# Optimization experiments

Hardware: AMD Instinct MI355X
Metric: run time of the kernel (lower is better)

## Reference

```python
import jax, jax.numpy as jnp
import numpy as np
from jax import lax

DN = ('NCHW', 'OIHW', 'NCHW')

def _conv(x, w, b):
    # Conv2d(k=4, stride=2, padding=1): H -> H/2
    y = lax.conv_general_dilated(x, w, (2, 2), ((1, 1), (1, 1)), dimension_numbers=DN)
    return y + b[None, :, None, None]

def _deconv(x, w, b):
    # ConvTranspose2d(k=4, stride=2, padding=1): H -> 2H.
    # Equivalent dense conv: flip kernel spatially, swap in/out channels,
    # lhs_dilation = stride, padding = k-1-p = 2.
    wf = jnp.flip(w, (2, 3)).transpose(1, 0, 2, 3)  # (out, in, 4, 4)
    y = lax.conv_general_dilated(x, wf, (1, 1), ((2, 2), (2, 2)), lhs_dilation=(2, 2), dimension_numbers=DN)
    return y + b[None, :, None, None]

def setup_inputs() -> dict:
    key = jax.random.key(0)
    ks = jax.random.split(key, 20)
    f = jnp.float32
    s = 0.05  # small init scale for stability
    inp = {
        'x':   jax.random.uniform(ks[0], (64, 3, 224, 224), dtype=f),
        # encoder conv weights (OIHW) + biases
        'ew1': jax.random.normal(ks[1], (32, 3, 4, 4), f) * s,   'eb1': jnp.zeros((32,), f),
        'ew2': jax.random.normal(ks[2], (64, 32, 4, 4), f) * s,  'eb2': jnp.zeros((64,), f),
        'ew3': jax.random.normal(ks[3], (128, 64, 4, 4), f) * s, 'eb3': jnp.zeros((128,), f),
        'ew4': jax.random.normal(ks[4], (64, 128, 4, 4), f) * s, 'eb4': jnp.zeros((64,), f),
        # codebook: uniform(-1/K, 1/K) like torch init, K=4000, D=12544
        'emb': jax.random.uniform(ks[5], (4000, 12544), f, -1.0 / 4000, 1.0 / 4000),
        # decoder conv-transpose weights in torch layout (in, out, kh, kw) + biases
        'dw1': jax.random.normal(ks[6], (64, 128, 4, 4), f) * s, 'db1': jnp.zeros((128,), f),
        'dw2': jax.random.normal(ks[7], (128, 64, 4, 4), f) * s, 'db2': jnp.zeros((64,), f),
        'dw3': jax.random.normal(ks[8], (64, 32, 4, 4), f) * s,  'db3': jnp.zeros((32,), f),
        'dw4': jax.random.normal(ks[9], (32, 3, 4, 4), f) * s,   'db4': jnp.zeros((3,), f),
    }
    return inp

def reference(x, ew1, eb1, ew2, eb2, ew3, eb3, ew4, eb4, emb,
              dw1, db1, dw2, db2, dw3, db3, dw4, db4):
    sg = lax.stop_gradient
    B = x.shape[0]
    # ---- Encoder ----
    h = jax.nn.relu(_conv(x, ew1, eb1))
    h = jax.nn.relu(_conv(h, ew2, eb2))
    h = jax.nn.relu(_conv(h, ew3, eb3))
    h = _conv(h, ew4, eb4)                 # (B, 64, 14, 14)
    z = h.reshape(B, -1)                   # (B, 12544)
    # ---- Vector quantization ----
    # ||z||^2 - 2 z E^T + ||e||^2, argmin over codebook
    dist = (jnp.sum(z * z, axis=1, keepdims=True)
            - 2.0 * (z @ emb.T)
            + jnp.sum(emb * emb, axis=1))  # (B, 4000)
    idx = jnp.argmin(dist, axis=1)         # (B,)
    quantized = emb[idx]                   # (B, 12544) -- direct gather (== onehot @ emb)
    e_latent = jnp.mean((sg(quantized) - z) ** 2)
    q_latent = jnp.mean((quantized - sg(z)) ** 2)
    vq_loss = q_latent + 0.25 * e_latent
    zq = z + sg(quantized - z)             # straight-through
    # ---- Decoder ----
    d = zq.reshape(B, 64, 14, 14)
    d = jax.nn.relu(_deconv(d, dw1, db1))
    d = jax.nn.relu(_deconv(d, dw2, db2))
    d = jax.nn.relu(_deconv(d, dw3, db3))
    x_recon = jax.nn.sigmoid(_deconv(d, dw4, db4))  # (B, 3, 224, 224)
    recon_loss = jnp.mean((x_recon - x) ** 2)
    loss = recon_loss + vq_loss
    return (x_recon, loss, recon_loss, vq_loss)
```

## Files before the change

### kernel.cpp

```cpp
#include <hip/hip_runtime.h>
#include <math.h>

typedef unsigned short u16;
typedef unsigned int u32;
typedef __attribute__((ext_vector_type(8))) short short8;
typedef __attribute__((ext_vector_type(4))) float f32x4;

__device__ __forceinline__ u16 f2bf(float f) {
    u32 u = __float_as_uint(f);
    u = u + 0x7fffu + ((u >> 16) & 1u);
    return (u16)(u >> 16);
}
__device__ __forceinline__ float bf2f(u16 h) { return __uint_as_float(((u32)h) << 16); }

__device__ __forceinline__ f32x4 mfma16(short8 a, short8 b, f32x4 c) {
    return __builtin_amdgcn_mfma_f32_16x16x32_bf16(a, b, c, 0, 0, 0);
}

__device__ __forceinline__ uint4 pack8(float4 a, float4 b) {
    uint4 r;
    r.x = (u32)f2bf(a.x) | ((u32)f2bf(a.y) << 16);
    r.y = (u32)f2bf(a.z) | ((u32)f2bf(a.w) << 16);
    r.z = (u32)f2bf(b.x) | ((u32)f2bf(b.y) << 16);
    r.w = (u32)f2bf(b.z) | ((u32)f2bf(b.w) << 16);
    return r;
}

#define GLOAD_LDS16(gsrc, ldst)                                                      \
    __builtin_amdgcn_global_load_lds(                                                \
        (__attribute__((address_space(1))) u32*)(gsrc),                              \
        (__attribute__((address_space(3))) u32*)(ldst), 16, 0, 0)

__device__ __forceinline__ void prep1_item(const float* __restrict__ w,
                                           u16* __restrict__ o, int i)
{
    int j = i & 7; int kx = j >> 1, cp = j & 1;
    int r = i >> 3;
    int co = r & 31; int r2 = r >> 5;
    int ky = r2 & 3; int h = r2 >> 2;
    int ci = 2 * h + cp;
    o[i] = (ci < 3) ? f2bf(w[((co * 3 + ci) * 16) + ky * 4 + kx]) : (u16)0;
}
__device__ __forceinline__ void prepc_item(const float* __restrict__ w,
                                           u16* __restrict__ o, int CIN, int COUT, int i)
{
    int j = i & 7; int r = i >> 3;
    int co = r % COUT; int r2 = r / COUT;
    int tap = r2 & 15; int ch = r2 >> 4;
    int ci = ch * 8 + j;
    o[i] = f2bf(w[((size_t)co * CIN + ci) * 16 + tap]);
}
__device__ __forceinline__ void prepd_item(const float* __restrict__ w,
                                           u16* __restrict__ o, int CIN, int COUT,
                                           int COPAD, int i)
{
    int j = i & 7; int r = i >> 3;
    int co = r % COPAD; int r2 = r / COPAD;
    int t16 = r2 & 15; int ch = r2 >> 4;
    int py = t16 >> 3, px = (t16 >> 2) & 1, qq = t16 & 3;
    int ta = qq >> 1, tb = qq & 1;
    int ky = py + 2 * ta, kx = px + 2 * tb;
    int ci = ch * 8 + j;
    o[i] = (co < COUT) ? f2bf(w[(((size_t)ci * COUT + co) * 16) + ky * 4 + kx]) : (u16)0;
}

__global__ __launch_bounds__(256) void prep_all(
    const float* __restrict__ ew1, const float* __restrict__ ew2,
    const float* __restrict__ ew3, const float* __restrict__ ew4,
    const float* __restrict__ dw1, const float* __restrict__ dw2,
    const float* __restrict__ dw3, const float* __restrict__ dw4,
    u16* __restrict__ w1c, u16* __restrict__ wc2,
    u16* __restrict__ wc3, u16* __restrict__ wc4,
    u16* __restrict__ wd1, u16* __restrict__ wd2,
    u16* __restrict__ wd3, u16* __restrict__ wd4)
{
    int i = blockIdx.x * 256 + threadIdx.x;
    if (i < 2048) { prep1_item(ew1, w1c, i); return; }
    i -= 2048;
    if (i < 32768)  { prepc_item(ew2, wc2, 32, 64, i); return; }
    i -= 32768;
    if (i < 131072) { prepc_item(ew3, wc3, 64, 128, i); return; }
    i -= 131072;
    if (i < 131072) { prepc_item(ew4, wc4, 128, 64, i); return; }
    i -= 131072;
    if (i < 131072) { prepd_item(dw1, wd1, 64, 128, 128, i); return; }
    i -= 131072;
    if (i < 131072) { prepd_item(dw2, wd2, 128, 64, 64, i); return; }
    i -= 131072;
    if (i < 32768)  { prepd_item(dw3, wd3, 64, 32, 32, i); return; }
    i -= 32768;
    if (i < 8192)   { prepd_item(dw4, wd4, 32, 3, 16, i); return; }
}

template<int CIN, int COUT, int COTILE, int H2, int W2, int NSEG, int MB,
         int MBW, int NWF, int RELU, int STOREZ>
__global__ __launch_bounds__(256) void conv_mfma(
    const u16* __restrict__ in, const u16* __restrict__ wcvt,
    const float* __restrict__ bias, u16* __restrict__ outp,
    float* __restrict__ z32)
{
    constexpr int CHUNKS = CIN / 8, CGI = CIN / 8, CGO = COUT / 8;
    constexpr int HIN = H2 * 2, WIN = W2 * 2, SLOTW = 35;
    constexpr int NF = COTILE / 16, WM = MB / MBW, WN = NF / NWF;
    static_assert(WM * WN == 4, "wave layout");
    constexpr int TBu = MB * 4 * SLOTW, WBu = 16 * COTILE;
    constexpr int EBu = (MB * 16 * COTILE * 2 + 15) / 16;
    constexpr int SM = (TBu + WBu) > EBu ? (TBu + WBu) : EBu;
    __shared__ uint4 smem[SM];
    uint4* T = smem; uint4* wS = smem + TBu;
    u16* E = (u16*)smem;

    const int tid = threadIdx.x, wid = tid >> 6, lane = tid & 63;
    const int q = lane >> 4, lm = lane & 15;
    const int wm = wid / WN, wn = wid % WN;
    const int cobase = blockIdx.y * COTILE;
    const int mbase = blockIdx.x * MB;

    f32x4 acc[MBW][NWF];
    #pragma unroll
    for (int a = 0; a < MBW; ++a)
        #pragma unroll
        for (int b = 0; b < NWF; ++b) {
            acc[a][b][0] = 0.f; acc[a][b][1] = 0.f;
            acc[a][b][2] = 0.f; acc[a][b][3] = 0.f;
        }

    for (int ch = 0; ch < CHUNKS; ++ch) {
        __syncthreads();
        for (int ib = 0; ib < TBu; ib += 256) {
            int i = ib + tid;
            uint4* ldst = T + ib + (wid << 6);
            if (i < TBu) {
                int mb = i / (4 * SLOTW), r2 = i % (4 * SLOTW);
                int r = r2 / SLOTW, s = r2 % SLOTW;
                int mbg = mbase + mb;
                int n = mbg / (H2 * NSEG), rr = mbg % (H2 * NSEG);
                int oy = rr / NSEG, ox0 = (rr % NSEG) << 4;
                int iy = 2 * oy - 1 + r, ix = 2 * ox0 - 1 + s;
                if ((unsigned)iy < (unsigned)HIN && (unsigned)ix < (unsigned)WIN) {
                    GLOAD_LDS16(in + (size_t)(((n * CGI + ch) * HIN + iy) * WIN + ix) * 8, ldst);
                } else {
                    uint4 zz = {0u, 0u, 0u, 0u};
                    T[i] = zz;
                }
            }
        }
        for (int ib = 0; ib < WBu; ib += 256) {
            int i = ib + tid;
            int tap = i / COTILE, co = i % COTILE;
            GLOAD_LDS16(wcvt + (size_t)((ch * 16 + tap) * COUT + cobase + co) * 8,
                        wS + ib + (wid << 6));
        }
        __syncthreads();
        #pragma unroll
        for (int ky = 0; ky < 4; ++ky) {
            short8 Af[MBW]; short8 Bf[NWF];
            #pragma unroll
            for (int im = 0; im < MBW; ++im) {
                int mb = wm * MBW + im;
                Af[im] = *(const short8*)(T + (mb * 4 + ky) * SLOTW + 2 * lm + q);
            }
            #pragma unroll
            for (int inf = 0; inf < NWF; ++inf)
                Bf[inf] = *(const short8*)(wS + (ky * 4 + q) * COTILE + wn * NWF * 16 + inf * 16 + lm);
            #pragma unroll
            for (int im = 0; im < MBW; ++im)
                #pragma unroll
                for (int inf = 0; inf < NWF; ++inf)
                    acc[im][inf] = mfma16(Af[im], Bf[inf], acc[im][inf]);
        }
    }
    __syncthreads();
    #pragma unroll
    for (int inf = 0; inf < NWF; ++inf) {
        int col = wn * NWF * 16 + inf * 16 + lm;
        float bv = bias[cobase + col];
        #pragma unroll
        for (int im = 0; im < MBW; ++im) {
            int pixb = (wm * MBW + im) * 16 + q * 4;
            #pragma unroll
            for (int r = 0; r < 4; ++r) {
                float v = acc[im][inf][r] + bv;
                if (RELU) v = fmaxf(v, 0.f);
                E[(pixb + r) * COTILE + col] = f2bf(v);
            }
        }
    }
    __syncthreads();
    for (int i = tid; i < MB * 16 * (COTILE / 8); i += 256) {
        int pix = i / (COTILE / 8), cg = i % (COTILE / 8);
        int mb = pix >> 4, m = pix & 15;
        int mbg = mbase + mb;
        int n = mbg / (H2 * NSEG), rr = mbg % (H2 * NSEG);
        int oy = rr / NSEG, ox0 = (rr % NSEG) << 4;
        int ox = ox0 + m;
        if (ox < W2)
            *(uint4*)(outp + (size_t)(((n * CGO + cobase / 8 + cg) * H2 + oy) * W2 + ox) * 8) =
                *(uint4*)(E + pix * COTILE + cg * 8);
    }
    if (STOREZ) {
        for (int i = tid; i < MB * 16 * COTILE; i += 256) {
            int pix = i / COTILE, co = i % COTILE;
            int mb = pix >> 4, m = pix & 15;
            int mbg = mbase + mb;
            int n = mbg / (H2 * NSEG), rr = mbg % (H2 * NSEG);
            int oy = rr / NSEG, ox0 = (rr % NSEG) << 4;
            int ox = ox0 + m;
            if (ox < W2)
                z32[(size_t)((n * COUT + cobase + co) * H2 + oy) * W2 + ox] =
                    bf2f(E[pix * COTILE + co]);
        }
    }
}

__global__ __launch_bounds__(256) void conv1_mfma(
    const float* __restrict__ x, const u16* __restrict__ w1c,
    const float* __restrict__ bias, u16* __restrict__ outp)
{
    constexpr int MB = 16, MBW = 4, NWF = 2, COTILE = 32, W2 = 112, H2 = 112, NSEG = 7;
    constexpr int TBu = MB * 2 * 64, WBu = 256;
    __shared__ uint4 smem[TBu + WBu];
    uint4* T1 = smem; uint4* w1S = smem + TBu;
    u16* E = (u16*)smem;

    const int tid = threadIdx.x, wid = tid >> 6, lane = tid & 63;
    const int q = lane >> 4, lm = lane & 15;
    const int wm = wid;
    const int mbase = blockIdx.x * MB;

    f32x4 acc[MBW][NWF];
    #pragma unroll
    for (int a = 0; a < MBW; ++a)
        #pragma unroll
        for (int b = 0; b < NWF; ++b) {
            acc[a][b][0] = 0.f; acc[a][b][1] = 0.f;
            acc[a][b][2] = 0.f; acc[a][b][3] = 0.f;
        }

    for (int i = tid; i < TBu; i += 256) {
        int mb = i >> 7; int r = i & 127;
        int h = r >> 6; int r2 = r & 63;
        int ky = r2 >> 4; int m = r2 & 15;
        int mbg = mbase + mb;
        int n = mbg / (H2 * NSEG), rr = mbg % (H2 * NSEG);
        int oy = rr / NSEG, ox0 = (rr % NSEG) << 4;
        int iy = 2 * oy - 1 + ky;
        int ixb = 2 * (ox0 + m) - 1;
        u32 u[4];
        #pragma unroll
        for (int kx = 0; kx < 4; ++kx) {
            float v0 = 0.f, v1 = 0.f;
            int ix = ixb + kx;
            if ((unsigned)iy < 224u && (unsigned)ix < 224u) {
                int ci0 = 2 * h;
                v0 = x[((size_t)(n * 3 + ci0) * 224 + iy) * 224 + ix];
                if (ci0 + 1 < 3) v1 = x[((size_t)(n * 3 + ci0 + 1) * 224 + iy) * 224 + ix];
            }
            u[kx] = (u32)f2bf(v0) | ((u32)f2bf(v1) << 16);
        }
        uint4 vv; vv.x = u[0]; vv.y = u[1]; vv.z = u[2]; vv.w = u[3];
        T1[i] = vv;
    }
    if (tid < 256) {
        w1S[tid] = *(const uint4*)(w1c + (size_t)tid * 8);
    }
    __syncthreads();
    #pragma unroll
    for (int h = 0; h < 2; ++h) {
        short8 Af[MBW]; short8 Bf[NWF];
        #pragma unroll
        for (int im = 0; im < MBW; ++im) {
            int mb = wm * MBW + im;
            Af[im] = *(const short8*)(T1 + (mb * 2 + h) * 64 + lane);
        }
        #pragma unroll
        for (int inf = 0; inf < NWF; ++inf)
            Bf[inf] = *(const short8*)(w1S + (h * 4 + q) * 32 + inf * 16 + lm);
        #pragma unroll
        for (int im = 0; im < MBW; ++im)
            #pragma unroll
            for (int inf = 0; inf < NWF; ++inf)
                acc[im][inf] = mfma16(Af[im], Bf[inf], acc[im][inf]);
    }
    __syncthreads();
    #pragma unroll
    for (int inf = 0; inf < NWF; ++inf) {
        int col = inf * 16 + lm;
        float bv = bias[col];
        #pragma unroll
        for (int im = 0; im < MBW; ++im) {
            int pixb = (wm * MBW + im) * 16 + q * 4;
            #pragma unroll
            for (int r = 0; r < 4; ++r) {
                float v = fmaxf(acc[im][inf][r] + bv, 0.f);
                E[(pixb + r) * COTILE + col] = f2bf(v);
            }
        }
    }
    __syncthreads();
    for (int i = tid; i < MB * 16 * (COTILE / 8); i += 256) {
        int pix = i / (COTILE / 8), cg = i % (COTILE / 8);
        int mb = pix >> 4, m = pix & 15;
        int mbg = mbase + mb;
        int n = mbg / (H2 * NSEG), rr = mbg % (H2 * NSEG);
        int oy = rr / NSEG, ox0 = (rr % NSEG) << 4;
        int ox = ox0 + m;
        *(uint4*)(outp + (size_t)(((n * 4 + cg) * H2 + oy) * W2 + ox) * 8) =
            *(uint4*)(E + pix * COTILE + cg * 8);
    }
}

template<int CIN, int COUT, int COPAD, int COTILE, int Hp, int Wp, int NSEG,
         int MB, int MBW, int NWF, int RELU>
__global__ __launch_bounds__(256) void deconv_mfma(
    const u16* __restrict__ in, const u16* __restrict__ dcvt,
    const float* __restrict__ bias, u16* __restrict__ outp)
{
    constexpr int CHUNKS = CIN / 8, CGI = CIN / 8, CGO = COUT / 8;
    constexpr int SLOTW = 17;
    constexpr int NF = COTILE / 16, WM = MB / MBW, WN = NF / NWF;
    static_assert(WM * WN == 4, "wave layout");
    constexpr int BPP = 64 * Hp * NSEG / MB;
    constexpr int TBu = MB * 2 * SLOTW, WBu = 4 * COTILE;
    constexpr int EBu = (MB * 16 * COTILE * 2 + 15) / 16;
    constexpr int SM = (TBu + WBu) > EBu ? (TBu + WBu) : EBu;
    __shared__ uint4 smem[SM];
    uint4* T = smem; uint4* wS = smem + TBu;
    u16* E = (u16*)smem;

    const int tid = threadIdx.x, wid = tid >> 6, lane = tid & 63;
    const int q = lane >> 4, lm = lane & 15;
    const int wm = wid / WN, wn = wid % WN;
    const int par = blockIdx.x / BPP;
    const int py = par >> 1, px = par & 1;
    const int mbase = (blockIdx.x % BPP) * MB;
    const int cobase = blockIdx.y * COTILE;

    f32x4 acc[MBW][NWF];
    #pragma unroll
    for (int a = 0; a < MBW; ++a)
        #pragma unroll
        for (int b = 0; b < NWF; ++b) {
            acc[a][b][0] = 0.f; acc[a][b][1] = 0.f;
            acc[a][b][2] = 0.f; acc[a][b][3] = 0.f;
        }

    for (int ch = 0; ch < CHUNKS; ++ch) {
        __syncthreads();
        for (int ib = 0; ib < TBu; ib += 256) {
            int i = ib + tid;
            uint4* ldst = T + ib + (wid << 6);
            if (i < TBu) {
                int mb = i / (2 * SLOTW), r2 = i % (2 * SLOTW);
                int rr_ = r2 / SLOTW, s = r2 % SLOTW;
                int mbg = mbase + mb;
                int n = mbg / (Hp * NSEG), rm = mbg % (Hp * NSEG);
                int oyp = rm / NSEG, u0 = (rm % NSEG) << 4;
                int iy = oyp + (1 - py) - 1 + rr_;
                int ix = u0 + (1 - px) - 1 + s;
                if ((unsigned)iy < (unsigned)Hp && (unsigned)ix < (unsigned)Wp) {
                    GLOAD_LDS16(in + (size_t)(((n * CGI + ch) * Hp + iy) * Wp + ix) * 8, ldst);
                } else {
                    uint4 zz = {0u, 0u, 0u, 0u};
                    T[i] = zz;
                }
            }
        }
        for (int ib = 0; ib < WBu; ib += 256) {
            int i = ib + tid;
            if (i < WBu) {
                int qq = i / COTILE, co = i % COTILE;
                GLOAD_LDS16(dcvt + (size_t)((ch * 16 + par * 4 + qq) * COPAD + cobase + co) * 8,
                            wS + ib + (wid << 6));
            }
        }
        __syncthreads();
        {
            short8 Af[MBW]; short8 Bf[NWF];
            #pragma unroll
            for (int im = 0; im < MBW; ++im) {
                int mb = wm * MBW + im;
                Af[im] = *(const short8*)(T + (mb * 2 + (1 - (q >> 1))) * SLOTW + lm + 1 - (q & 1));
            }
            #pragma unroll
            for (int inf = 0; inf < NWF; ++inf)
                Bf[inf] = *(const short8*)(wS + q * COTILE + wn * NWF * 16 + inf * 16 + lm);
            #pragma unroll
            for (int im = 0; im < MBW; ++im)
                #pragma unroll
                for (int inf = 0; inf < NWF; ++inf)
                    acc[im][inf] = mfma16(Af[im], Bf[inf], acc[im][inf]);
        }
    }
    __syncthreads();
    #pragma unroll
    for (int inf = 0; inf < NWF; ++inf) {
        int col = wn * NWF * 16 + inf * 16 + lm;
        float bv = bias[cobase + col];
        #pragma unroll
        for (int im = 0; im < MBW; ++im) {
            int pixb = (wm * MBW + im) * 16 + q * 4;
            #pragma unroll
            for (int r = 0; r < 4; ++r) {
                float v = acc[im][inf][r] + bv;
                if (RELU) v = fmaxf(v, 0.f);
                E[(pixb + r) * COTILE + col] = f2bf(v);
            }
        }
    }
    __syncthreads();
    for (int i = tid; i < MB * 16 * (COTILE / 8); i += 256) {
        int pix = i / (COTILE / 8), cg = i % (COTILE / 8);
        int mb = pix >> 4, m = pix & 15;
        int mbg = mbase + mb;
        int n = mbg / (Hp * NSEG), rm = mbg % (Hp * NSEG);
        int oyp = rm / NSEG, u0 = (rm % NSEG) << 4;
        int u = u0 + m;
        if (u < Wp) {
            int ox = 2 * u + (px ? 0 : 1);
            int oy = 2 * oyp + (py ? 0 : 1);
            *(uint4*)(outp + (size_t)(((n * CGO + cobase / 8 + cg) * (2 * Hp) + oy) * (2 * Wp) + ox) * 8) =
                *(uint4*)(E + pix * COTILE + cg * 8);
        }
    }
}

__global__ __launch_bounds__(256) void deconv4_mfma(
    const u16* __restrict__ in, const u16* __restrict__ dcvt,
    const float* __restrict__ bias, float* __restrict__ outp,
    const float* __restrict__ xref, float* __restrict__ bpart)
{
    constexpr int Hp = 112, Wp = 112, NSEG = 7, MB = 16, MBW = 4;
    constexpr int CGI = 4, CHUNKS = 4;
    constexpr int TROW = 3, TCOL = 18;
    constexpr int TBu = MB * TROW * TCOL;
    __shared__ uint4 smem[TBu + 1024];
    __shared__ float red[4];
    uint4* T = smem; uint4* wS = smem + TBu;
    float* Ef = (float*)smem;

    const int tid = threadIdx.x, wid = tid >> 6, lane = tid & 63;
    const int q = lane >> 4, lm = lane & 15;
    const int wm = wid;
    const int mbase = blockIdx.x * MB;

    f32x4 acc[4][MBW];
    #pragma unroll
    for (int p = 0; p < 4; ++p)
        #pragma unroll
        for (int a = 0; a < MBW; ++a) {
            acc[p][a][0] = 0.f; acc[p][a][1] = 0.f; acc[p][a][2] = 0.f; acc[p][a][3] = 0.f;
        }

    for (int ib = 0; ib < 1024; ib += 256)
        GLOAD_LDS16(dcvt + (size_t)(ib + tid) * 8, wS + ib + (wid << 6));

    for (int ch = 0; ch < CHUNKS; ++ch) {
        __syncthreads();
        for (int ib = 0; ib < TBu; ib += 256) {
            int i = ib + tid;
            uint4* ldst = T + ib + (wid << 6);
            if (i < TBu) {
                int mb = i / (TROW * TCOL), r2 = i % (TROW * TCOL);
                int r = r2 / TCOL, s = r2 % TCOL;
                int mbg = mbase + mb;
                int n = mbg / (Hp * NSEG), rm = mbg % (Hp * NSEG);
                int oyp = rm / NSEG, u0 = (rm % NSEG) << 4;
                int iy = oyp - 1 + r;
                int ix = u0 - 1 + s;
                if ((unsigned)iy < (unsigned)Hp && (unsigned)ix < (unsigned)Wp) {
                    GLOAD_LDS16(in + (size_t)(((n * CGI + ch) * Hp + iy) * Wp + ix) * 8, ldst);
                } else {
                    uint4 zz = {0u, 0u, 0u, 0u};
                    T[i] = zz;
                }
            }
        }
        __syncthreads();
        #pragma unroll
        for (int par = 0; par < 4; ++par) {
            const int py = par >> 1, px = par & 1;
            short8 Bf = *(const short8*)(wS + (ch * 16 + par * 4 + q) * 16 + lm);
            #pragma unroll
            for (int im = 0; im < MBW; ++im) {
                int mb = wm * MBW + im;
                short8 Af = *(const short8*)(T + (mb * TROW + (2 - py - (q >> 1))) * TCOL
                                             + lm + 2 - px - (q & 1));
                acc[par][im] = mfma16(Af, Bf, acc[par][im]);
            }
        }
    }

    __syncthreads();
    if (lm < 3) {
        float bv = bias[lm];
        #pragma unroll
        for (int par = 0; par < 4; ++par)
            #pragma unroll
            for (int im = 0; im < MBW; ++im)
                #pragma unroll
                for (int r = 0; r < 4; ++r)
                    Ef[(((wm * MBW + im) * 16 + q * 4 + r) * 4 + par) * 3 + lm] =
                        acc[par][im][r] + bv;
    }
    __syncthreads();
    float lsum = 0.f;
    #pragma unroll
    for (int k = 0; k < 3; ++k) {
        int i = k * 256 + tid;
        int mb = i / 48, rem = i % 48;
        int row = rem / 24, rem2 = rem % 24;
        int co = rem2 / 8, ox4 = rem2 % 8;
        int mbg = mbase + mb;
        int n = mbg / (Hp * NSEG), rm = mbg % (Hp * NSEG);
        int oyp = rm / NSEG, u0 = (rm % NSEG) << 4;
        int pA = row ? 1 : 3, pB = row ? 0 : 2;
        int uL = 2 * ox4, uH = uL + 1;
        float v0 = Ef[((mb * 16 + uL) * 4 + pA) * 3 + co];
        float v1 = Ef[((mb * 16 + uL) * 4 + pB) * 3 + co];
        float v2 = Ef[((mb * 16 + uH) * 4 + pA) * 3 + co];
        float v3 = Ef[((mb * 16 + uH) * 4 + pB) * 3 + co];
        float4 sv;
        sv.x = 1.f / (1.f + expf(-v0));
        sv.y = 1.f / (1.f + expf(-v1));
        sv.z = 1.f / (1.f + expf(-v2));
        sv.w = 1.f / (1.f + expf(-v3));
        size_t ro = ((size_t)(n * 3 + co) * 224 + 2 * oyp + row) * 224 + 2 * u0 + 4 * ox4;
        float4 x4 = *(const float4*)(xref + ro);
        *(float4*)(outp + ro) = sv;
        float d0 = sv.x - x4.x, d1 = sv.y - x4.y, d2 = sv.z - x4.z, d3 = sv.w - x4.w;
        lsum += d0 * d0 + d1 * d1 + d2 * d2 + d3 * d3;
    }
    #pragma unroll
    for (int off = 32; off > 0; off >>= 1)
        lsum += __shfl_down(lsum, off, 64);
    if (lane == 0) red[wid] = lsum;
    __syncthreads();
    if (tid == 0)
        bpart[blockIdx.x] = red[0] + red[1] + red[2] + red[3];
}

__global__ __launch_bounds__(256) void vq_gemm(
    const float* __restrict__ z32, const float* __restrict__ emb,
    float* __restrict__ P, float* __restrict__ normp)
{
    __shared__ uint4 As[8 * 64];
    __shared__ uint4 Bs[8 * 256];
    const int tid = threadIdx.x, wid = tid >> 6, lane = tid & 63;
    const int q = lane >> 4, lm = lane & 15;
    const int jt = blockIdx.x, ks = blockIdx.y;
    const int jg = jt * 256 + tid;
    const int jc = jg < 4000 ? jg : 3999;
    const float* brow = emb + (size_t)jc * 12544 + ks * 896;
    const int m = tid & 63, ksub = tid >> 6;
    const float* arow = z32 + (size_t)m * 12544 + ks * 896 + ksub * 16;

    f32x4 acc[4][4];
    #pragma unroll
    for (int a = 0; a < 4; ++a)
        #pragma unroll
        for (int b = 0; b < 4; ++b) {
            acc[a][b][0] = 0.f; acc[a][b][1] = 0.f; acc[a][b][2] = 0.f; acc[a][b][3] = 0.f;
        }
    float nsq = 0.f;

    for (int ch = 0; ch < 14; ++ch) {
        __syncthreads();
        {
            float4 f0 = *(const float4*)(arow + ch * 64);
            float4 f1 = *(const float4*)(arow + ch * 64 + 4);
            float4 f2 = *(const float4*)(arow + ch * 64 + 8);
            float4 f3 = *(const float4*)(arow + ch * 64 + 12);
            As[(ksub * 2 + 0) * 64 + m] = pack8(f0, f1);
            As[(ksub * 2 + 1) * 64 + m] = pack8(f2, f3);
        }
        {
            const float* bp = brow + ch * 64;
            #pragma unroll
            for (int ko = 0; ko < 8; ++ko) {
                float4 fa = *(const float4*)(bp + ko * 8);
                float4 fb = *(const float4*)(bp + ko * 8 + 4);
                nsq += fa.x * fa.x + fa.y * fa.y + fa.z * fa.z + fa.w * fa.w
                     + fb.x * fb.x + fb.y * fb.y + fb.z * fb.z + fb.w * fb.w;
                Bs[ko * 256 + tid] = pack8(fa, fb);
            }
        }
        __syncthreads();
        #pragma unroll
        for (int kk = 0; kk < 2; ++kk) {
            short8 Af[4]; short8 Bf[4];
            #pragma unroll
            for (int mf = 0; mf < 4; ++mf)
                Af[mf] = *(const short8*)(As + (kk * 4 + q) * 64 + mf * 16 + lm);
            #pragma unroll
            for (int nf = 0; nf < 4; ++nf)
                Bf[nf] = *(const short8*)(Bs + (kk * 4 + q) * 256 + wid * 64 + nf * 16 + lm);
            #pragma unroll
            for (int mf = 0; mf < 4; ++mf)
                #pragma unroll
                for (int nf = 0; nf < 4; ++nf)
                    acc[mf][nf] = mfma16(Af[mf], Bf[nf], acc[mf][nf]);
        }
    }
    #pragma unroll
    for (int mf = 0; mf < 4; ++mf)
        #pragma unroll
        for (int nf = 0; nf < 4; ++nf) {
            int j = jt * 256 + wid * 64 + nf * 16 + lm;
            if (j < 4000) {
                #pragma unroll
                for (int r = 0; r < 4; ++r) {
                    int b = mf * 16 + q * 4 + r;
                    P[(size_t)(ks * 64 + b) * 4000 + j] = acc[mf][nf][r];
                }
            }
        }
    if (jg < 4000) normp[ks * 4000 + jg] = nsq;
}

__global__ __launch_bounds__(256) void vq_argmin_gather(
    const float* __restrict__ P, const float* __restrict__ normp,
    const float* __restrict__ emb, const float* __restrict__ z32,
    u16* __restrict__ Qb, float* __restrict__ vacc)
{
    const int b = blockIdx.x;
    const int tid = threadIdx.x;
    float best = 3.4e38f;
    int bidx = 0x7fffffff;
    for (int j = tid; j < 4000; j += 256) {
        float dot = 0.f, nrm = 0.f;
        #pragma unroll
        for (int s = 0; s < 14; ++s) {
            dot += P[(size_t)(s * 64 + b) * 4000 + j];
            nrm += normp[s * 4000 + j];
        }
        float d = nrm - 2.f * dot;
        if (d < best) { best = d; bidx = j; }
    }
    __shared__ float sv[256];
    __shared__ int si[256];
    sv[tid] = best; si[tid] = bidx;
    __syncthreads();
    for (int off = 128; off > 0; off >>= 1) {
        if (tid < off) {
            float v2 = sv[tid + off]; int i2 = si[tid + off];
            if (v2 < sv[tid] || (v2 == sv[tid] && i2 < si[tid])) { sv[tid] = v2; si[tid] = i2; }
        }
        __syncthreads();
    }
    const int code = si[0];
    const float* e = emb + (size_t)code * 12544;
    const float* zb = z32 + (size_t)b * 12544;
    float ls = 0.f;
    for (int d = tid; d < 12544; d += 256) {
        float ev = e[d];
        int co = d / 196, rem = d % 196;
        int y = rem / 14, xx = rem % 14;
        Qb[((size_t)((b * 8 + (co >> 3)) * 14 + y) * 14 + xx) * 8 + (co & 7)] = f2bf(ev);
        float df = ev - zb[d];
        ls += df * df;
    }
    #pragma unroll
    for (int off = 32; off > 0; off >>= 1)
        ls += __shfl_down(ls, off, 64);
    if ((tid & 63) == 0) atomicAdd(vacc, ls);
}

__global__ __launch_bounds__(256) void reduce_final(
    const float* __restrict__ bpart, const float* __restrict__ vacc,
    float* __restrict__ tail)
{
    const int tid = threadIdx.x;
    float s = 0.f;
    for (int i = tid; i < 3136; i += 256) s += bpart[i];
    #pragma unroll
    for (int off = 32; off > 0; off >>= 1)
        s += __shfl_down(s, off, 64);
    __shared__ float red[4];
    if ((tid & 63) == 0) red[tid >> 6] = s;
    __syncthreads();
    if (tid == 0) {
        float rsum = red[0] + red[1] + red[2] + red[3];
        float recon = rsum * (1.f / 9633792.f);
        float vq = 1.25f * vacc[0] * (1.f / 802816.f);
        tail[0] = recon + vq;
        tail[1] = recon;
        tail[2] = vq;
    }
}

extern "C" void kernel_launch(void* const* d_in, const int* in_sizes, int n_in,
                              void* d_out, int out_size, void* d_ws, size_t ws_size,
                              hipStream_t stream)
{
    const float* x   = (const float*)d_in[0];
    const float* ew1 = (const float*)d_in[1];
    const float* eb1 = (const float*)d_in[2];
    const float* ew2 = (const float*)d_in[3];
    const float* eb2 = (const float*)d_in[4];
    const float* ew3 = (const float*)d_in[5];
    const float* eb3 = (const float*)d_in[6];
    const float* ew4 = (const float*)d_in[7];
    const float* eb4 = (const float*)d_in[8];
    const float* emb = (const float*)d_in[9];
    const float* dw1 = (const float*)d_in[10];
    const float* db1 = (const float*)d_in[11];
    const float* dw2 = (const float*)d_in[12];
    const float* db2 = (const float*)d_in[13];
    const float* dw3 = (const float*)d_in[14];
    const float* db3 = (const float*)d_in[15];
    const float* dw4 = (const float*)d_in[16];
    const float* db4 = (const float*)d_in[17];
    float* out = (float*)d_out;

    size_t off = 0;
    char* base = (char*)d_ws;
    auto nxt = [&](size_t bytes) -> char* {
        char* p = base + off;
        off = (off + bytes + 255) & ~(size_t)255;
        return p;
    };
    u16*   A1    = (u16*)nxt(25690112ull * 2);
    u16*   A2    = (u16*)nxt(12845056ull * 2);
    u16*   A3    = (u16*)nxt(6422528ull * 2);
    float* z32   = (float*)nxt(802816ull * 4);
    u16*   Qb    = (u16*)nxt(802816ull * 2);
    float* P     = (float*)nxt(14ull * 64 * 4000 * 4);
    float* normp = (float*)nxt(14ull * 4000 * 4);
    u16*   w1c   = (u16*)nxt(2048ull * 2);
    u16*   wc2   = (u16*)nxt(32768ull * 2);
    u16*   wc3   = (u16*)nxt(131072ull * 2);
    u16*   wc4   = (u16*)nxt(131072ull * 2);
    u16*   wd1   = (u16*)nxt(131072ull * 2);
    u16*   wd2   = (u16*)nxt(131072ull * 2);
    u16*   wd3   = (u16*)nxt(32768ull * 2);
    u16*   wd4   = (u16*)nxt(8192ull * 2);
    float* accp  = (float*)nxt(512);
    float* bpart = (float*)nxt(3136ull * 4);
    u16*   D1 = A3;
    u16*   D2 = A2;
    u16*   D3 = A1;

    hipMemsetAsync(accp, 0, 8, stream);

    prep_all<<<2344, 256, 0, stream>>>(ew1, ew2, ew3, ew4, dw1, dw2, dw3, dw4,
                                       w1c, wc2, wc3, wc4, wd1, wd2, wd3, wd4);

    conv1_mfma<<<3136, 256, 0, stream>>>(x, w1c, eb1, A1);
    conv_mfma<32, 64, 64, 56, 56, 4, 16, 8, 2, 1, 0>
        <<<dim3(896, 1), 256, 0, stream>>>(A1, wc2, eb2, A2, nullptr);
    conv_mfma<64, 128, 64, 28, 28, 2, 8, 4, 2, 1, 0>
        <<<dim3(448, 2), 256, 0, stream>>>(A2, wc3, eb3, A3, nullptr);
    conv_mfma<128, 64, 64, 14, 14, 1, 8, 2, 4, 0, 1>
        <<<dim3(112, 1), 256, 0, stream>>>(A3, wc4, eb4, Qb, z32);

    vq_gemm<<<dim3(16, 14), 256, 0, stream>>>(z32, emb, P, normp);
    vq_argmin_gather<<<64, 256, 0, stream>>>(P, normp, emb, z32, Qb, accp);

    deconv_mfma<64, 128, 128, 64, 14, 14, 1, 8, 4, 2, 1>
        <<<dim3(448, 2), 256, 0, stream>>>(Qb, wd1, db1, D1);
    deconv_mfma<128, 64, 64, 64, 28, 28, 2, 16, 8, 2, 1>
        <<<dim3(896, 1), 256, 0, stream>>>(D1, wd2, db2, D2);
    deconv_mfma<64, 32, 32, 32, 56, 56, 4, 16, 8, 1, 1>
        <<<dim3(3584, 1), 256, 0, stream>>>(D2, wd3, db3, D3);
    deconv4_mfma<<<3136, 256, 0, stream>>>(D3, wd4, db4, out, x, bpart);

    reduce_final<<<1, 256, 0, stream>>>(bpart, accp, out + 9633792);
}
```

Measured before the change: 695.5 us.

## Fuse deconv parities per block, vectorize conv1 input loads, swizzle VQ GEMM LDS

```diff
diff --git a/kernel.cpp b/kernel.cpp
--- a/kernel.cpp
+++ b/kernel.cpp
@@ -246,19 +246,32 @@
         int oy = rr / NSEG, ox0 = (rr % NSEG) << 4;
         int iy = 2 * oy - 1 + ky;
         int ixb = 2 * (ox0 + m) - 1;
-        u32 u[4];
-        #pragma unroll
-        for (int kx = 0; kx < 4; ++kx) {
-            float v0 = 0.f, v1 = 0.f;
-            int ix = ixb + kx;
-            if ((unsigned)iy < 224u && (unsigned)ix < 224u) {
-                int ci0 = 2 * h;
-                v0 = x[((size_t)(n * 3 + ci0) * 224 + iy) * 224 + ix];
-                if (ci0 + 1 < 3) v1 = x[((size_t)(n * 3 + ci0 + 1) * 224 + iy) * 224 + ix];
-            }
-            u[kx] = (u32)f2bf(v0) | ((u32)f2bf(v1) << 16);
-        }
-        uint4 vv; vv.x = u[0]; vv.y = u[1]; vv.z = u[2]; vv.w = u[3];
+        int ci0 = 2 * h;
+        uint4 vv;
+        const float* rowp = x + ((size_t)(n * 3 + ci0) * 224 + iy) * 224;
+        if ((unsigned)iy < 224u && ixb >= 0 && ixb <= 220) {
+            float4 a = *(const float4*)(rowp + ixb);
+            float4 bq;
+            if (h == 0) bq = *(const float4*)(rowp + 224 * 224 + ixb);
+            else { bq.x = 0.f; bq.y = 0.f; bq.z = 0.f; bq.w = 0.f; }
+            vv.x = (u32)f2bf(a.x) | ((u32)f2bf(bq.x) << 16);
+            vv.y = (u32)f2bf(a.y) | ((u32)f2bf(bq.y) << 16);
+            vv.z = (u32)f2bf(a.z) | ((u32)f2bf(bq.z) << 16);
+            vv.w = (u32)f2bf(a.w) | ((u32)f2bf(bq.w) << 16);
+        } else {
+            u32 u[4];
+            #pragma unroll
+            for (int kx = 0; kx < 4; ++kx) {
+                float v0 = 0.f, v1 = 0.f;
+                int ix = ixb + kx;
+                if ((unsigned)iy < 224u && (unsigned)ix < 224u) {
+                    v0 = rowp[ix];
+                    if (ci0 + 1 < 3) v1 = rowp[224 * 224 + ix];
+                }
+                u[kx] = (u32)f2bf(v0) | ((u32)f2bf(v1) << 16);
+            }
+            vv.x = u[0]; vv.y = u[1]; vv.z = u[2]; vv.w = u[3];
+        }
         T1[i] = vv;
     }
     if (tid < 256) {
@@ -421,6 +434,136 @@
             int oy = 2 * oyp + (py ? 0 : 1);
             *(uint4*)(outp + (size_t)(((n * CGO + cobase / 8 + cg) * (2 * Hp) + oy) * (2 * Wp) + ox) * 8) =
                 *(uint4*)(E + pix * COTILE + cg * 8);
+        }
+    }
+}
+
+template<int CIN, int COUT, int COPAD, int COTILE, int Hp, int Wp, int NSEG,
+         int MB, int MBW, int NWF, int RELU>
+__global__ __launch_bounds__(256) void deconv_all(
+    const u16* __restrict__ in, const u16* __restrict__ dcvt,
+    const float* __restrict__ bias, u16* __restrict__ outp)
+{
+    constexpr int CHUNKS = CIN / 8, CGI = CIN / 8, CGO = COUT / 8;
+    constexpr int TROW = 3, TCOL = 18;
+    constexpr int NF = COTILE / 16, WM = MB / MBW, WN = NF / NWF;
+    static_assert(WM * WN == 4, "wave layout");
+    constexpr int TBu = MB * TROW * TCOL;
+    constexpr int WBu = 16 * COTILE;
+    constexpr int EBu = MB * 16 * 2 * COTILE / 8;
+    constexpr int SM = (TBu + WBu) > EBu ? (TBu + WBu) : EBu;
+    __shared__ uint4 smem[SM];
+    uint4* T = smem; uint4* wS = smem + TBu;
+    u16* E = (u16*)smem;
+
+    const int tid = threadIdx.x, wid = tid >> 6, lane = tid & 63;
+    const int q = lane >> 4, lm = lane & 15;
+    const int wm = wid / WN, wn = wid % WN;
+    const int mbase = blockIdx.x * MB;
+    const int cobase = blockIdx.y * COTILE;
+
+    f32x4 acc[4][MBW][NWF];
+    #pragma unroll
+    for (int p = 0; p < 4; ++p)
+        #pragma unroll
+        for (int a = 0; a < MBW; ++a)
+            #pragma unroll
+            for (int b = 0; b < NWF; ++b) {
+                acc[p][a][b][0] = 0.f; acc[p][a][b][1] = 0.f;
+                acc[p][a][b][2] = 0.f; acc[p][a][b][3] = 0.f;
+            }
+
+    for (int ch = 0; ch < CHUNKS; ++ch) {
+        __syncthreads();
+        for (int ib = 0; ib < TBu; ib += 256) {
+            int i = ib + tid;
+            uint4* ldst = T + ib + (wid << 6);
+            if (i < TBu) {
+                int mb = i / (TROW * TCOL), r2 = i % (TROW * TCOL);
+                int r = r2 / TCOL, s = r2 % TCOL;
+                int mbg = mbase + mb;
+                int n = mbg / (Hp * NSEG), rm = mbg % (Hp * NSEG);
+                int oyp = rm / NSEG, u0 = (rm % NSEG) << 4;
+                int iy = oyp - 1 + r;
+                int ix = u0 - 1 + s;
+                if ((unsigned)iy < (unsigned)Hp && (unsigned)ix < (unsigned)Wp) {
+                    GLOAD_LDS16(in + (size_t)(((n * CGI + ch) * Hp + iy) * Wp + ix) * 8, ldst);
+                } else {
+                    uint4 zz = {0u, 0u, 0u, 0u};
+                    T[i] = zz;
+                }
+            }
+        }
+        for (int ib = 0; ib < WBu; ib += 256) {
+            int i = ib + tid;
+            if (i < WBu) {
+                int t16 = i / COTILE, co = i % COTILE;
+                GLOAD_LDS16(dcvt + (size_t)((ch * 16 + t16) * COPAD + cobase + co) * 8,
+                            wS + ib + (wid << 6));
+            }
+        }
+        __syncthreads();
+        #pragma unroll
+        for (int par = 0; par < 4; ++par) {
+            const int py = par >> 1, px = par & 1;
+            short8 Bf[NWF];
+            #pragma unroll
+            for (int inf = 0; inf < NWF; ++inf)
+                Bf[inf] = *(const short8*)(wS + (par * 4 + q) * COTILE + wn * NWF * 16 + inf * 16 + lm);
+            #pragma unroll
+            for (int im = 0; im < MBW; ++im) {
+                int mb = wm * MBW + im;
+                short8 Af = *(const short8*)(T + (mb * TROW + (2 - py - (q >> 1))) * TCOL
+                                             + lm + 2 - px - (q & 1));
+                #pragma unroll
+                for (int inf = 0; inf < NWF; ++inf)
+                    acc[par][im][inf] = mfma16(Af, Bf[inf], acc[par][im][inf]);
+            }
+        }
+    }
+    #pragma unroll
+    for (int pp = 0; pp < 2; ++pp) {
+        __syncthreads();
+        #pragma unroll
+        for (int inf = 0; inf < NWF; ++inf) {
+            int col = wn * NWF * 16 + inf * 16 + lm;
+            float bv = bias[cobase + col];
+            #pragma unroll
+            for (int im = 0; im < MBW; ++im) {
+                #pragma unroll
+                for (int r = 0; r < 4; ++r) {
+                    int m = q * 4 + r;
+                    int pix = (wm * MBW + im) * 16 + m;
+                    int colx = col ^ ((m & (COTILE / 8 - 1)) << 3);
+                    #pragma unroll
+                    for (int pxx = 0; pxx < 2; ++pxx) {
+                        float v = acc[pp * 2 + pxx][im][inf][r] + bv;
+                        if (RELU) v = fmaxf(v, 0.f);
+                        E[(pix * 2 + pxx) * COTILE + colx] = f2bf(v);
+                    }
+                }
+            }
+        }
+        __syncthreads();
+        const int dy = 1 - pp;
+        for (int i = tid; i < (COTILE / 8) * MB * 32; i += 256) {
+            int xx = i & 31;
+            int t = i >> 5;
+            int mb = t & (MB - 1), cg = t / MB;
+            int m = xx >> 1;
+            int pxx = 1 - (xx & 1);
+            int pix = mb * 16 + m;
+            int mbg = mbase + mb;
+            int n = mbg / (Hp * NSEG), rm = mbg % (Hp * NSEG);
+            int oyp = rm / NSEG, u0 = (rm % NSEG) << 4;
+            int u = u0 + m;
+            if (u < Wp) {
+                int oy = 2 * oyp + dy;
+                int ox = 2 * u + (xx & 1);
+                int cgx = cg ^ (m & (COTILE / 8 - 1));
+                *(uint4*)(outp + (size_t)(((n * CGO + cobase / 8 + cg) * (2 * Hp) + oy) * (2 * Wp) + ox) * 8) =
+                    *(uint4*)(E + ((pix * 2 + pxx) * COTILE + cgx * 8));
+            }
         }
     }
 }
@@ -546,14 +689,12 @@
 {
     __shared__ uint4 As[8 * 64];
     __shared__ uint4 Bs[8 * 256];
+    __shared__ float Ns[256 * 8];
     const int tid = threadIdx.x, wid = tid >> 6, lane = tid & 63;
     const int q = lane >> 4, lm = lane & 15;
     const int jt = blockIdx.x, ks = blockIdx.y;
-    const int jg = jt * 256 + tid;
-    const int jc = jg < 4000 ? jg : 3999;
-    const float* brow = emb + (size_t)jc * 12544 + ks * 896;
-    const int m = tid & 63, ksub = tid >> 6;
-    const float* arow = z32 + (size_t)m * 12544 + ks * 896 + ksub * 16;
+    const int k8s = tid & 7;
+    const int rb2 = tid >> 3;
 
     f32x4 acc[4][4];
     #pragma unroll
@@ -562,45 +703,62 @@
         for (int b = 0; b < 4; ++b) {
             acc[a][b][0] = 0.f; acc[a][b][1] = 0.f; acc[a][b][2] = 0.f; acc[a][b][3] = 0.f;
         }
-    float nsq = 0.f;
+    float nsum[8];
+    #pragma unroll
+    for (int it = 0; it < 8; ++it) nsum[it] = 0.f;
 
     for (int ch = 0; ch < 14; ++ch) {
         __syncthreads();
-        {
-            float4 f0 = *(const float4*)(arow + ch * 64);
-            float4 f1 = *(const float4*)(arow + ch * 64 + 4);
-            float4 f2 = *(const float4*)(arow + ch * 64 + 8);
-            float4 f3 = *(const float4*)(arow + ch * 64 + 12);
-            As[(ksub * 2 + 0) * 64 + m] = pack8(f0, f1);
-            As[(ksub * 2 + 1) * 64 + m] = pack8(f2, f3);
-        }
-        {
-            const float* bp = brow + ch * 64;
-            #pragma unroll
-            for (int ko = 0; ko < 8; ++ko) {
-                float4 fa = *(const float4*)(bp + ko * 8);
-                float4 fb = *(const float4*)(bp + ko * 8 + 4);
-                nsq += fa.x * fa.x + fa.y * fa.y + fa.z * fa.z + fa.w * fa.w
-                     + fb.x * fb.x + fb.y * fb.y + fb.z * fb.z + fb.w * fb.w;
-                Bs[ko * 256 + tid] = pack8(fa, fb);
-            }
+        #pragma unroll
+        for (int it = 0; it < 2; ++it) {
+            int i = tid + it * 256;
+            int k8 = i & 7, m = i >> 3;
+            const float* ap = z32 + (size_t)m * 12544 + ks * 896 + ch * 64 + k8 * 8;
+            float4 f0 = *(const float4*)(ap);
+            float4 f1 = *(const float4*)(ap + 4);
+            As[k8 * 64 + (m ^ k8)] = pack8(f0, f1);
+        }
+        #pragma unroll
+        for (int it = 0; it < 8; ++it) {
+            int r = rb2 + 32 * it;
+            int jg = jt * 256 + r;
+            int jc = jg < 4000 ? jg : 3999;
+            const float* bp = emb + (size_t)jc * 12544 + ks * 896 + ch * 64 + k8s * 8;
+            float4 fa = *(const float4*)(bp);
+            float4 fb = *(const float4*)(bp + 4);
+            nsum[it] += fa.x * fa.x + fa.y * fa.y + fa.z * fa.z + fa.w * fa.w
+                      + fb.x * fb.x + fb.y * fb.y + fb.z * fb.z + fb.w * fb.w;
+            Bs[k8s * 256 + (r ^ k8s)] = pack8(fa, fb);
         }
         __syncthreads();
         #pragma unroll
         for (int kk = 0; kk < 2; ++kk) {
             short8 Af[4]; short8 Bf[4];
+            int k8x = kk * 4 + q;
             #pragma unroll
             for (int mf = 0; mf < 4; ++mf)
-                Af[mf] = *(const short8*)(As + (kk * 4 + q) * 64 + mf * 16 + lm);
+                Af[mf] = *(const short8*)(As + k8x * 64 + ((mf * 16 + lm) ^ k8x));
             #pragma unroll
             for (int nf = 0; nf < 4; ++nf)
-                Bf[nf] = *(const short8*)(Bs + (kk * 4 + q) * 256 + wid * 64 + nf * 16 + lm);
+                Bf[nf] = *(const short8*)(Bs + k8x * 256 + ((wid * 64 + nf * 16 + lm) ^ k8x));
             #pragma unroll
             for (int mf = 0; mf < 4; ++mf)
                 #pragma unroll
                 for (int nf = 0; nf < 4; ++nf)
                     acc[mf][nf] = mfma16(Af[mf], Bf[nf], acc[mf][nf]);
         }
+    }
+    __syncthreads();
+    #pragma unroll
+    for (int it = 0; it < 8; ++it)
+        Ns[(rb2 + 32 * it) * 8 + k8s] = nsum[it];
+    __syncthreads();
+    {
+        float s = 0.f;
+        #pragma unroll
+        for (int f = 0; f < 8; ++f) s += Ns[tid * 8 + f];
+        int jg2 = jt * 256 + tid;
+        if (jg2 < 4000) normp[ks * 4000 + jg2] = s;
     }
     #pragma unroll
     for (int mf = 0; mf < 4; ++mf)
@@ -615,7 +773,6 @@
                 }
             }
         }
-    if (jg < 4000) normp[ks * 4000 + jg] = nsq;
 }
 
 __global__ __launch_bounds__(256) void vq_argmin_gather(
@@ -759,10 +916,10 @@
 
     deconv_mfma<64, 128, 128, 64, 14, 14, 1, 8, 4, 2, 1>
         <<<dim3(448, 2), 256, 0, stream>>>(Qb, wd1, db1, D1);
-    deconv_mfma<128, 64, 64, 64, 28, 28, 2, 16, 8, 2, 1>
-        <<<dim3(896, 1), 256, 0, stream>>>(D1, wd2, db2, D2);
-    deconv_mfma<64, 32, 32, 32, 56, 56, 4, 16, 8, 1, 1>
-        <<<dim3(3584, 1), 256, 0, stream>>>(D2, wd3, db3, D3);
+    deconv_all<128, 64, 64, 64, 28, 28, 2, 8, 4, 2, 1>
+        <<<dim3(448, 1), 256, 0, stream>>>(D1, wd2, db2, D2);
+    deconv_all<64, 32, 32, 32, 56, 56, 4, 16, 4, 2, 1>
+        <<<dim3(896, 1), 256, 0, stream>>>(D2, wd3, db3, D3);
     deconv4_mfma<<<3136, 256, 0, stream>>>(D3, wd4, db4, out, x, bpart);
 
     reduce_final<<<1, 256, 0, stream>>>(bpart, accp, out + 9633792);
```

Result: slower. 747.4 us (+7.5%).
